# Kernel optimization log

Hardware: AMD Instinct MI355X
Metric: run time of the kernel (lower is better)

The kernel has to match this reference:

```python
import jax, jax.numpy as jnp
import numpy as np

B, S, H, NH, DIS = 8, 512, 512, 8, 32
HD = H // NH  # head_dim = 64


def setup_inputs() -> dict:
    key = jax.random.key(0)
    ks = jax.random.split(key, 9)
    sc = 0.05
    return {
        "x": jax.random.normal(ks[0], (B, S, H), jnp.float32),
        "rel_distance": jax.random.randint(ks[1], (B, S, 2 * S), 0, DIS, jnp.int64),
        "mask": jnp.zeros((B, S, 2 * S), jnp.bool_),
        "query_pos_embedding": jax.random.normal(ks[2], (DIS, H), jnp.float32) * sc,
        "key_pos_embedding": jax.random.normal(ks[3], (DIS, H), jnp.float32) * sc,
        "value_pos_embedding": jax.random.normal(ks[4], (DIS, H), jnp.float32) * sc,
        "Wq": jax.random.normal(ks[5], (H, H), jnp.float32) * sc,
        "Wk": jax.random.normal(ks[6], (2 * H, H), jnp.float32) * sc,
        "Wv": jax.random.normal(ks[7], (2 * H, H), jnp.float32) * sc,
        "Wo": jax.random.normal(ks[8], (H, H), jnp.float32) * sc,
    }


def reference(x, rel_distance, mask, query_pos_embedding, key_pos_embedding,
              value_pos_embedding, Wq, Wk, Wv, Wo):
    b, s, _ = x.shape
    scale = jnp.sqrt(jnp.asarray(HD, x.dtype))

    # projections (torch Linear: y = x @ W.T)
    q = (x @ Wq.T).reshape(b, s, NH, HD).transpose(0, 2, 1, 3)        # [B,h,S,d]
    k = (x @ Wk.T).reshape(b, 2 * s, NH, HD).transpose(0, 2, 1, 3)    # [B,h,2S,d]
    v = (x @ Wv.T).reshape(b, 2 * s, NH, HD).transpose(0, 2, 1, 3)    # [B,h,2S,d]

    rel = jnp.broadcast_to(rel_distance[:, None], (b, NH, s, 2 * s))  # [B,h,S,2S]

    # relative-position weights via gather along distance axis
    q_emb = query_pos_embedding.reshape(DIS, NH, HD)                  # [n,h,d]
    qpw_full = jnp.einsum('bhsd,nhd->bhsn', q, q_emb)                 # [B,h,S,n]
    qpw = jnp.take_along_axis(qpw_full, rel, axis=3)                  # [B,h,S,2S]

    k_emb = key_pos_embedding.reshape(DIS, NH, HD)
    kpw_full = jnp.einsum('bhkd,nhd->bhkn', k, k_emb)                 # [B,h,2S,n]
    kpw = jnp.take_along_axis(kpw_full, rel.transpose(0, 1, 3, 2), axis=3)  # [B,h,2S,S]
    kpw = kpw.transpose(0, 1, 3, 2)                                   # [B,h,S,2S]

    scores = (jnp.einsum('bhsd,bhkd->bhsk', q, k) + qpw + kpw) / scale
    scores = jnp.where(mask[:, None], -jnp.inf, scores)
    probs = jax.nn.softmax(scores, axis=-1)                           # [B,h,S,2S]

    # scatter-add probs into distance buckets: [B,h,S,n]
    bi = jnp.arange(b)[:, None, None, None]
    hi = jnp.arange(NH)[None, :, None, None]
    si = jnp.arange(s)[None, None, :, None]
    vdw = jnp.zeros((b, NH, s, DIS), probs.dtype).at[bi, hi, si, rel].add(probs)

    v_emb = value_pos_embedding.reshape(DIS, NH, HD)                  # [n,h,d]
    out = jnp.einsum('bhsk,bhkd->bhsd', probs, v) \
        + jnp.einsum('bhsn,nhd->bhsd', vdw, v_emb)                    # [B,h,S,d]
    out = out.transpose(0, 2, 1, 3).reshape(b, s, H)
    return out @ Wo.T
```

## Files before the change

kernel.cpp:

```cpp
#include <hip/hip_runtime.h>
#include <math.h>

#define Bc 8
#define Sc 512
#define Hc 512
#define NHc 8
#define HDc 64
#define DISc 32
#define S2c 1024

typedef __attribute__((ext_vector_type(8))) short bf16x8;
typedef __attribute__((ext_vector_type(4))) float f32x4;
#define MFMA16(a, b, c) __builtin_amdgcn_mfma_f32_16x16x32_bf16(a, b, c, 0, 0, 0)

__device__ __forceinline__ unsigned short f2bf(float f) {
  unsigned u = __float_as_uint(f);
  return (unsigned short)((u + 0x7fffu + ((u >> 16) & 1u)) >> 16);
}
__device__ __forceinline__ float b2f(unsigned short u) {
  return __uint_as_float((unsigned)u << 16);
}
__device__ __forceinline__ bf16x8 ldb16x8(const unsigned short* p) {
  union { uint4 u; bf16x8 s; } cv;
  cv.u = *(const uint4*)p;
  return cv.s;
}

__global__ __launch_bounds__(256) void cvt5_k(
    const float* __restrict__ x, const float* __restrict__ wq,
    const float* __restrict__ wk, const float* __restrict__ wv,
    const float* __restrict__ wo, unsigned short* __restrict__ x16,
    unsigned short* __restrict__ w16q, unsigned short* __restrict__ w16k,
    unsigned short* __restrict__ w16v, unsigned short* __restrict__ w16o) {
  int i = blockIdx.x * 256 + threadIdx.x;
  const float* src; unsigned short* dst; int off; float sc = 1.f;
  if (i < 524288)      { src = x;  dst = x16;  off = i; }
  else if (i < 589824) { src = wq; dst = w16q; off = i - 524288; sc = 0.125f; }
  else if (i < 720896) { src = wk; dst = w16k; off = i - 589824; }
  else if (i < 851968) { src = wv; dst = w16v; off = i - 720896; }
  else                 { src = wo; dst = w16o; off = i - 851968; }
  float4 v = ((const float4*)src)[off];
  ushort4 u;
  u.x = f2bf(v.x * sc); u.y = f2bf(v.y * sc);
  u.z = f2bf(v.z * sc); u.w = f2bf(v.w * sc);
  ((ushort4*)dst)[off] = u;
}

__global__ __launch_bounds__(256) void pack_k(const int* __restrict__ rel,
                                              const unsigned char* __restrict__ mask,
                                              unsigned char* __restrict__ pk8) {
  int i = blockIdx.x * 256 + threadIdx.x;
  const int* rp = rel + i * 16;
  uint4 mu = *(const uint4*)(mask + i * 16);
  const unsigned char* mb = (const unsigned char*)&mu;
  uint4 o;
  unsigned* ow = (unsigned*)&o;
#pragma unroll
  for (int g = 0; g < 4; ++g) {
    int4 r4 = ((const int4*)rp)[g];
    unsigned b0 = ((unsigned)r4.x & 31u) | (mb[g * 4 + 0] ? 0x80u : 0u);
    unsigned b1 = ((unsigned)r4.y & 31u) | (mb[g * 4 + 1] ? 0x80u : 0u);
    unsigned b2 = ((unsigned)r4.z & 31u) | (mb[g * 4 + 2] ? 0x80u : 0u);
    unsigned b3 = ((unsigned)r4.w & 31u) | (mb[g * 4 + 3] ? 0x80u : 0u);
    ow[g] = b0 | (b1 << 8) | (b2 << 16) | (b3 << 24);
  }
  *(uint4*)(pk8 + i * 16) = o;
}

__global__ __launch_bounds__(256) void wemb_k(
    const float* __restrict__ qpe, const float* __restrict__ kpe,
    const float* __restrict__ Wq, const float* __restrict__ Wk,
    unsigned short* __restrict__ wqp, unsigned short* __restrict__ wkp) {
  const int bid = blockIdx.x;
  const int cc = bid & 3, unit = bid >> 2;
  const int c0 = cc << 7;
  const int t = threadIdx.x;
  const float* emb; const float* Wsrc; unsigned short* outp; int rowbase, h;
  if (unit < 8) {
    h = unit; emb = qpe; Wsrc = Wq + (size_t)(h * 64) * 512; outp = wqp; rowbase = h * 32;
  } else {
    int u = unit - 8; int e = u >> 3; h = u & 7;
    emb = kpe; Wsrc = Wk + (size_t)(e * 512 + h * 64) * 512; outp = wkp;
    rowbase = e * 256 + h * 32;
  }
  __shared__ float es[32][65];
  __shared__ float wsh[64][132];
  {
    int n = t >> 3, d4 = (t & 7) << 3;
    float4 v0 = *(const float4*)(emb + (size_t)n * 512 + h * 64 + d4);
    float4 v1 = *(const float4*)(emb + (size_t)n * 512 + h * 64 + d4 + 4);
    *(float4*)&es[n][d4] = v0;
    *(float4*)&es[n][d4 + 4] = v1;
  }
#pragma unroll
  for (int p = 0; p < 8; ++p) {
    int slot = t + (p << 8);
    int d = slot >> 5, c4 = (slot & 31) << 2;
    *(float4*)&wsh[d][c4] = *(const float4*)(Wsrc + (size_t)d * 512 + c0 + c4);
  }
  __syncthreads();
  const int n = t >> 3, cb = (t & 7) << 4;
  float acc[16] = {};
#pragma unroll
  for (int d = 0; d < 64; ++d) {
    float ev = es[n][d];
    float4 w0 = *(const float4*)&wsh[d][cb];
    float4 w1 = *(const float4*)&wsh[d][cb + 4];
    float4 w2 = *(const float4*)&wsh[d][cb + 8];
    float4 w3 = *(const float4*)&wsh[d][cb + 12];
    acc[0] = fmaf(ev, w0.x, acc[0]);   acc[1] = fmaf(ev, w0.y, acc[1]);
    acc[2] = fmaf(ev, w0.z, acc[2]);   acc[3] = fmaf(ev, w0.w, acc[3]);
    acc[4] = fmaf(ev, w1.x, acc[4]);   acc[5] = fmaf(ev, w1.y, acc[5]);
    acc[6] = fmaf(ev, w1.z, acc[6]);   acc[7] = fmaf(ev, w1.w, acc[7]);
    acc[8] = fmaf(ev, w2.x, acc[8]);   acc[9] = fmaf(ev, w2.y, acc[9]);
    acc[10] = fmaf(ev, w2.z, acc[10]); acc[11] = fmaf(ev, w2.w, acc[11]);
    acc[12] = fmaf(ev, w3.x, acc[12]); acc[13] = fmaf(ev, w3.y, acc[13]);
    acc[14] = fmaf(ev, w3.z, acc[14]); acc[15] = fmaf(ev, w3.w, acc[15]);
  }
  unsigned short* orow = outp + (size_t)(rowbase + n) * 512 + c0 + cb;
#pragma unroll
  for (int j = 0; j < 16; ++j) orow[j] = f2bf(acc[j] * 0.125f);
}

__global__ __launch_bounds__(256, 4) void gemmqkv_k(
    const unsigned short* __restrict__ A,
    const unsigned short* __restrict__ wq, const unsigned short* __restrict__ wqp,
    const unsigned short* __restrict__ wk, const unsigned short* __restrict__ wkp,
    const unsigned short* __restrict__ wv,
    unsigned short* __restrict__ q16h, unsigned short* __restrict__ qpw16,
    unsigned short* __restrict__ kb16, unsigned short* __restrict__ kpw16,
    unsigned short* __restrict__ vT16) {
  const int t = threadIdx.x;
  const int w = t >> 6, lane = t & 63, ln = lane & 15, qd = lane >> 4;
  const int wm = (w >> 1) << 5, wn = (w & 1) << 5;
  const int m0 = blockIdx.y << 6, n0 = blockIdx.x << 6;
  __shared__ unsigned short As[64 * 72];
  __shared__ unsigned short Bs[64 * 72];
  const unsigned short* Bb;
  if (n0 < 512)        Bb = wq  + (size_t)n0 * 512;
  else if (n0 < 768)   Bb = wqp + (size_t)(n0 - 512) * 512;
  else if (n0 < 1792)  Bb = wk  + (size_t)(n0 - 768) * 512;
  else if (n0 < 2304)  Bb = wkp + (size_t)(n0 - 1792) * 512;
  else                 Bb = wv  + (size_t)(n0 - 2304) * 512;
  const int r0 = t >> 3, c8 = (t & 7) << 3;
  const unsigned short* ga = A + (size_t)(m0 + r0) * 512 + c8;
  const unsigned short* gb = Bb + (size_t)r0 * 512 + c8;
  const size_t half = (size_t)32 * 512;
  uint4 va0 = *(const uint4*)ga, va1 = *(const uint4*)(ga + half);
  uint4 vb0 = *(const uint4*)gb, vb1 = *(const uint4*)(gb + half);
  f32x4 z = {0.f, 0.f, 0.f, 0.f};
  f32x4 acc[2][2] = {{z, z}, {z, z}};
  for (int k0 = 0; k0 < 512; k0 += 64) {
    *(uint4*)&As[r0 * 72 + c8] = va0;
    *(uint4*)&As[(r0 + 32) * 72 + c8] = va1;
    *(uint4*)&Bs[r0 * 72 + c8] = vb0;
    *(uint4*)&Bs[(r0 + 32) * 72 + c8] = vb1;
    __syncthreads();
    if (k0 + 64 < 512) {
      va0 = *(const uint4*)(ga + k0 + 64);
      va1 = *(const uint4*)(ga + half + k0 + 64);
      vb0 = *(const uint4*)(gb + k0 + 64);
      vb1 = *(const uint4*)(gb + half + k0 + 64);
    }
#pragma unroll
    for (int kk = 0; kk < 64; kk += 32) {
      bf16x8 a0 = ldb16x8(&As[(wm + ln) * 72 + kk + qd * 8]);
      bf16x8 a1 = ldb16x8(&As[(wm + 16 + ln) * 72 + kk + qd * 8]);
      bf16x8 b0 = ldb16x8(&Bs[(wn + ln) * 72 + kk + qd * 8]);
      bf16x8 b1 = ldb16x8(&Bs[(wn + 16 + ln) * 72 + kk + qd * 8]);
      acc[0][0] = MFMA16(a0, b0, acc[0][0]);
      acc[0][1] = MFMA16(a0, b1, acc[0][1]);
      acc[1][0] = MFMA16(a1, b0, acc[1][0]);
      acc[1][1] = MFMA16(a1, b1, acc[1][1]);
    }
    __syncthreads();
  }
#pragma unroll
  for (int tm = 0; tm < 2; ++tm)
#pragma unroll
    for (int tn = 0; tn < 2; ++tn)
#pragma unroll
      for (int r = 0; r < 4; ++r) {
        int m = m0 + wm + tm * 16 + qd * 4 + r;
        int n = n0 + wn + tn * 16 + ln;
        unsigned short v16 = f2bf(acc[tm][tn][r]);
        int bb = m >> 9, s = m & 511;
        if (n0 < 512) {
          int hh = (n >> 6) & 7, d = n & 63;
          q16h[((size_t)(bb * 8 + hh) * 512 + s) * 64 + d] = v16;
        } else if (n0 < 768) {
          int n2 = n - 512, hh = n2 >> 5, nn = n2 & 31;
          qpw16[((size_t)(bb * 8 + hh) * 512 + s) * 32 + nn] = v16;
        } else if (n0 < 1792) {
          int n2 = n - 768, e = n2 >> 9, hh = (n2 >> 6) & 7, d = n2 & 63;
          int k2 = 2 * s + e;
          kb16[((size_t)(bb * 8 + hh) * 1024 + k2) * 64 + d] = v16;
        } else if (n0 < 2304) {
          int n2 = n - 1792, e = n2 >> 8, hh = (n2 >> 5) & 7, nn = n2 & 31;
          int k2 = 2 * s + e;
          kpw16[((size_t)(bb * 8 + hh) * 1024 + k2) * 32 + nn] = v16;
        } else {
          int n2 = n - 2304, e = n2 >> 9, hh = (n2 >> 6) & 7, d = n2 & 63;
          int k2 = 2 * s + e;
          vT16[((size_t)(bb * 8 + hh) * 64 + d) * 1024 + k2] = v16;
        }
      }
}

__global__ __launch_bounds__(256) void gemmo_k(
    const unsigned short* __restrict__ A, const unsigned short* __restrict__ Bw,
    float* __restrict__ out) {
  const int t = threadIdx.x;
  const int w = t >> 6, lane = t & 63, ln = lane & 15, qd = lane >> 4;
  const int wm = (w >> 1) << 6, wn = (w & 1) << 5;
  const int m0 = blockIdx.y << 7, n0 = blockIdx.x << 6;
  __shared__ unsigned short As[128 * 72];
  __shared__ unsigned short Bs[64 * 72];
  const int r0 = t >> 3, c8 = (t & 7) << 3;
  const unsigned short* ga = A + (size_t)(m0 + r0) * 512 + c8;
  const unsigned short* gb = Bw + (size_t)(n0 + r0) * 512 + c8;
  const size_t rs = (size_t)32 * 512;
  uint4 va0 = *(const uint4*)ga;
  uint4 va1 = *(const uint4*)(ga + rs);
  uint4 va2 = *(const uint4*)(ga + 2 * rs);
  uint4 va3 = *(const uint4*)(ga + 3 * rs);
  uint4 vb0 = *(const uint4*)gb;
  uint4 vb1 = *(const uint4*)(gb + rs);
  f32x4 z = {0.f, 0.f, 0.f, 0.f};
  f32x4 a00 = z, a01 = z, a10 = z, a11 = z;
  f32x4 a20 = z, a21 = z, a30 = z, a31 = z;
  for (int k0 = 0; k0 < 512; k0 += 64) {
    *(uint4*)&As[(r0) * 72 + c8] = va0;
    *(uint4*)&As[(r0 + 32) * 72 + c8] = va1;
    *(uint4*)&As[(r0 + 64) * 72 + c8] = va2;
    *(uint4*)&As[(r0 + 96) * 72 + c8] = va3;
    *(uint4*)&Bs[(r0) * 72 + c8] = vb0;
    *(uint4*)&Bs[(r0 + 32) * 72 + c8] = vb1;
    __syncthreads();
    if (k0 + 64 < 512) {
      va0 = *(const uint4*)(ga + k0 + 64);
      va1 = *(const uint4*)(ga + rs + k0 + 64);
      va2 = *(const uint4*)(ga + 2 * rs + k0 + 64);
      va3 = *(const uint4*)(ga + 3 * rs + k0 + 64);
      vb0 = *(const uint4*)(gb + k0 + 64);
      vb1 = *(const uint4*)(gb + rs + k0 + 64);
    }
#pragma unroll
    for (int kk = 0; kk < 64; kk += 32) {
      bf16x8 af0 = ldb16x8(&As[(wm + ln) * 72 + kk + qd * 8]);
      bf16x8 af1 = ldb16x8(&As[(wm + 16 + ln) * 72 + kk + qd * 8]);
      bf16x8 af2 = ldb16x8(&As[(wm + 32 + ln) * 72 + kk + qd * 8]);
      bf16x8 af3 = ldb16x8(&As[(wm + 48 + ln) * 72 + kk + qd * 8]);
      bf16x8 bf0 = ldb16x8(&Bs[(wn + ln) * 72 + kk + qd * 8]);
      bf16x8 bf1 = ldb16x8(&Bs[(wn + 16 + ln) * 72 + kk + qd * 8]);
      a00 = MFMA16(af0, bf0, a00); a01 = MFMA16(af0, bf1, a01);
      a10 = MFMA16(af1, bf0, a10); a11 = MFMA16(af1, bf1, a11);
      a20 = MFMA16(af2, bf0, a20); a21 = MFMA16(af2, bf1, a21);
      a30 = MFMA16(af3, bf0, a30); a31 = MFMA16(af3, bf1, a31);
    }
    __syncthreads();
  }
  float* ob = out + (size_t)(m0 + wm + qd * 4) * 512 + n0 + wn + ln;
#define ST(tm, tn, reg)                                            \
  _Pragma("unroll") for (int r = 0; r < 4; ++r)                    \
      ob[(size_t)((tm) * 16 + r) * 512 + (tn) * 16] = reg[r];
  ST(0, 0, a00) ST(0, 1, a01) ST(1, 0, a10) ST(1, 1, a11)
  ST(2, 0, a20) ST(2, 1, a21) ST(3, 0, a30) ST(3, 1, a31)
#undef ST
}

__global__ __launch_bounds__(512, 4) void attn6_k(
    const unsigned short* __restrict__ q16h, const unsigned short* __restrict__ kb16,
    const unsigned short* __restrict__ vT16, const unsigned short* __restrict__ qpw16,
    const unsigned short* __restrict__ kpw16, const unsigned char* __restrict__ pk8,
    const float* __restrict__ v_emb, unsigned short* __restrict__ attn16) {
  const int bid = blockIdx.x;
  const int b = bid & 7;
  const int h = (bid >> 3) & 7;
  const int qb = ((bid >> 6) & 7) << 6;
  const int t = threadIdx.x;
  const int w = t >> 6;
  const int g = w >> 2;
  const int ws4 = w & 3;
  const int lane = t & 63;
  const int ln = lane & 15;
  const int qd = lane >> 4;

  __shared__ __align__(16) char smem[52736];
  unsigned char*  pkt  = (unsigned char*)smem;
  unsigned short* kpws = (unsigned short*)(smem + 10240);
  unsigned short* q32s = (unsigned short*)(smem + 19456);
  unsigned short* pbuf = (unsigned short*)(smem + 24064);
  unsigned long long* vdwm64 = (unsigned long long*)(smem + 34304);
  float*          accbuf = (float*)smem;
  unsigned short* vest   = (unsigned short*)(smem + 19456);
  unsigned short* vdwb   = (unsigned short*)(smem + 24576);

  for (int i = t; i < 4 * 16 * 36; i += 512) vdwm64[i] = 0ull;
  if (t < 256) {
    int row = t >> 2, c8 = (t & 3) << 3;
    *(uint4*)&q32s[row * 36 + c8] =
        *(const uint4*)(qpw16 + ((size_t)((b * 8 + h) * 512 + qb) + row) * 32 + c8);
  }
  const unsigned short* kbase = kb16 + (size_t)(b * 8 + h) * 65536;
  const unsigned short* vbase = vT16 + (size_t)(b * 8 + h) * 65536;
  bf16x8 aQ[2];
  {
    const unsigned short* qsrc =
        q16h + ((size_t)((b * 8 + h) * 512 + qb + ws4 * 16 + ln)) * 64;
    aQ[0] = ldb16x8(qsrc + qd * 8);
    aQ[1] = ldb16x8(qsrc + 32 + qd * 8);
  }
  f32x4 z = {0.f, 0.f, 0.f, 0.f};
  f32x4 acc[4] = {z, z, z, z};

  const int u = t & 255, gg = t >> 8;
  const int qr = u >> 2, cg = (u & 3) << 4;
  const int kc8 = (u & 3) << 3;
  const unsigned char* pks = pk8 + ((size_t)(b * 512 + qb + qr)) * 1024 + (gg << 9);
  const unsigned short* kps =
      kpw16 + ((size_t)((b * 8 + h) * 1024) + (gg << 9) + qr) * 32 + kc8;
  unsigned char* pt_w = pkt + gg * 5120 + qr * 80 + cg;
  unsigned short* kp_w = kpws + gg * 2304 + qr * 36 + kc8;

  uint4 pv = *(const uint4*)(pks + cg);
  uint4 kv = *(const uint4*)kps;

  for (int kti = 0; kti < 8; ++kti) {
    *(uint4*)pt_w = pv;
    *(uint4*)kp_w = kv;
    __syncthreads();
    if (kti < 7) {
      pv = *(const uint4*)(pks + ((kti + 1) << 6) + cg);
      kv = *(const uint4*)(kps + ((size_t)(kti + 1) << 11));
    }
    const int kt0 = (kti + g * 8) << 6;

    f32x4 sc4[4];
#pragma unroll
    for (int t4 = 0; t4 < 4; ++t4) {
      f32x4 c = z;
      c = MFMA16(aQ[0], ldb16x8(kbase + (size_t)(kt0 + t4 * 16 + ln) * 64 + qd * 8), c);
      c = MFMA16(aQ[1], ldb16x8(kbase + (size_t)(kt0 + t4 * 16 + ln) * 64 + 32 + qd * 8), c);
      sc4[t4] = c;
    }

    unsigned char* pt_ = pkt + g * 5120;
    unsigned short* kp_ = kpws + g * 2304;
#pragma unroll
    for (int hf = 0; hf < 2; ++hf) {
#pragma unroll
      for (int r = 0; r < 4; ++r) {
#pragma unroll
        for (int t4h = 0; t4h < 2; ++t4h) {
          int t4 = hf * 2 + t4h;
          int row_l = ws4 * 16 + qd * 4 + r;
          int kl = t4 * 16 + ln;
          unsigned um = pt_[row_l * 80 + kl];
          int rd = um & 31;
          float s = sc4[t4][r] + b2f(q32s[row_l * 36 + rd]) + b2f(kp_[kl * 36 + rd]);
          float p = (um & 0x80u) ? 0.f : __expf(s);
          atomicAdd(&vdwm64[ws4 * 576 + (qd * 4 + r) * 36 + rd],
                    (unsigned long long)(p * 67108864.0f));
          pbuf[w * 640 + (qd * 4 + r) * 40 + t4h * 16 + ln] = f2bf(p);
        }
      }
      bf16x8 ah = ldb16x8(&pbuf[w * 640 + ln * 40 + qd * 8]);
#pragma unroll
      for (int dt = 0; dt < 4; ++dt)
        acc[dt] = MFMA16(ah, ldb16x8(vbase + (size_t)(dt * 16 + ln) * 1024 + kt0 + hf * 32 + qd * 8), acc[dt]);
    }
    __syncthreads();
  }

  if (t < 256) {
    int n = t >> 3, d0 = (t & 7) << 3;
    const float* src = v_emb + ((size_t)n << 9) + (h << 6) + d0;
    float4 f0 = *(const float4*)src;
    float4 f1 = *(const float4*)(src + 4);
    vest[(d0 + 0) * 40 + n] = f2bf(f0.x); vest[(d0 + 1) * 40 + n] = f2bf(f0.y);
    vest[(d0 + 2) * 40 + n] = f2bf(f0.z); vest[(d0 + 3) * 40 + n] = f2bf(f0.w);
    vest[(d0 + 4) * 40 + n] = f2bf(f1.x); vest[(d0 + 5) * 40 + n] = f2bf(f1.y);
    vest[(d0 + 6) * 40 + n] = f2bf(f1.z); vest[(d0 + 7) * 40 + n] = f2bf(f1.w);
  } else {
    int row = lane >> 2, n0 = (lane & 3) << 3;
    float vv[8];
#pragma unroll
    for (int j = 0; j < 8; ++j)
      vv[j] = (float)vdwm64[ws4 * 576 + row * 36 + n0 + j] * 1.4901161193847656e-8f;
    ushort4 u0, u1;
    u0.x = f2bf(vv[0]); u0.y = f2bf(vv[1]); u0.z = f2bf(vv[2]); u0.w = f2bf(vv[3]);
    u1.x = f2bf(vv[4]); u1.y = f2bf(vv[5]); u1.z = f2bf(vv[6]); u1.w = f2bf(vv[7]);
    *(ushort4*)&vdwb[ws4 * 640 + row * 40 + n0] = u0;
    *(ushort4*)&vdwb[ws4 * 640 + row * 40 + n0 + 4] = u1;
  }
  __syncthreads();

  if (g == 1) {
    bf16x8 av = ldb16x8(&vdwb[ws4 * 640 + ln * 40 + qd * 8]);
#pragma unroll
    for (int dt = 0; dt < 4; ++dt)
      acc[dt] = MFMA16(av, ldb16x8(&vest[(dt * 16 + ln) * 40 + qd * 8]), acc[dt]);
#pragma unroll
    for (int r = 0; r < 4; ++r)
#pragma unroll
      for (int dt = 0; dt < 4; ++dt)
        accbuf[ws4 * 1088 + (qd * 4 + r) * 68 + dt * 16 + ln] = acc[dt][r];
  }
  __syncthreads();

  if (g == 0) {
    float inv[4];
#pragma unroll
    for (int r = 0; r < 4; ++r) {
      unsigned long long lu = 0ull;
#pragma unroll
      for (int n = 0; n < 32; ++n)
        lu += vdwm64[ws4 * 576 + (qd * 4 + r) * 36 + n];
      inv[r] = 67108864.0f / (float)lu;
    }
    unsigned short* obase =
        attn16 + ((size_t)(b * 512 + qb + ws4 * 16 + qd * 4)) * 512 + (h << 6);
#pragma unroll
    for (int r = 0; r < 4; ++r)
#pragma unroll
      for (int dt = 0; dt < 4; ++dt) {
        float v = (acc[dt][r] + accbuf[ws4 * 1088 + (qd * 4 + r) * 68 + dt * 16 + ln]) * inv[r];
        obase[(size_t)r * 512 + dt * 16 + ln] = f2bf(v);
      }
  }
}

extern "C" void kernel_launch(void* const* d_in, const int* in_sizes, int n_in,
                              void* d_out, int out_size, void* d_ws, size_t ws_size,
                              hipStream_t stream) {
  const float* x = (const float*)d_in[0];
  const int* rel = (const int*)d_in[1];
  const unsigned char* mask = (const unsigned char*)d_in[2];
  const float* qpe = (const float*)d_in[3];
  const float* kpe = (const float*)d_in[4];
  const float* vpe = (const float*)d_in[5];
  const float* Wq = (const float*)d_in[6];
  const float* Wk = (const float*)d_in[7];
  const float* Wv = (const float*)d_in[8];
  const float* Wo = (const float*)d_in[9];
  float* out = (float*)d_out;

  unsigned short* u = (unsigned short*)d_ws;
  unsigned short* x16    = u;
  unsigned short* w16q   = x16 + 2097152;
  unsigned short* w16k   = w16q + 262144;
  unsigned short* w16v   = w16k + 524288;
  unsigned short* w16o   = w16v + 524288;
  unsigned short* wqp16  = w16o + 262144;
  unsigned short* wkp16  = wqp16 + 131072;
  unsigned short* q16h   = wkp16 + 262144;
  unsigned short* qpw16  = q16h + 2097152;
  unsigned short* kb16   = qpw16 + 1048576;
  unsigned short* kpw16  = kb16 + 4194304;
  unsigned short* vT16   = kpw16 + 2097152;
  unsigned short* attn16 = vT16 + 4194304;
  unsigned char* pk8 = (unsigned char*)(attn16 + 2097152);

  pack_k<<<1024, 256, 0, stream>>>(rel, mask, pk8);
  cvt5_k<<<3584, 256, 0, stream>>>(x, Wq, Wk, Wv, Wo, x16, w16q, w16k, w16v, w16o);
  wemb_k<<<96, 256, 0, stream>>>(qpe, kpe, Wq, Wk, wqp16, wkp16);
  gemmqkv_k<<<dim3(52, 64), 256, 0, stream>>>(x16, w16q, wqp16, w16k, wkp16, w16v,
                                              q16h, qpw16, kb16, kpw16, vT16);
  attn6_k<<<512, 512, 0, stream>>>(q16h, kb16, vT16, qpw16, kpw16, pk8, vpe, attn16);
  gemmo_k<<<dim3(8, 32), 256, 0, stream>>>(attn16, w16o, out);
}
```

Before: 217.1 us.

## Split attention key range across four wave groups with 32-row query tiles

The attention kernel now assigns 32 query rows per block instead of 64 and launches 1024 blocks. The 8 waves form 4 groups, each covering a quarter of the 1024 keys, where before 2 groups each covered half. Partial output accumulators from three groups go through shared memory and are summed by group 0. This raises grid size and per-row key-split parallelism, which should help occupancy and latency hiding. The cost is extra cross-group reduction traffic and the K/V fragments being reloaded by twice as many blocks.

After: 222.2 us. 1.02x slower.

```diff
diff --git a/kernel.cpp b/kernel.cpp
--- a/kernel.cpp
+++ b/kernel.cpp
@@ -269,7 +269,7 @@
 #undef ST
 }
 
-__global__ __launch_bounds__(512, 4) void attn6_k(
+__global__ __launch_bounds__(512, 4) void attn7_k(
     const unsigned short* __restrict__ q16h, const unsigned short* __restrict__ kb16,
     const unsigned short* __restrict__ vT16, const unsigned short* __restrict__ qpw16,
     const unsigned short* __restrict__ kpw16, const unsigned char* __restrict__ pk8,
@@ -277,75 +277,81 @@
   const int bid = blockIdx.x;
   const int b = bid & 7;
   const int h = (bid >> 3) & 7;
-  const int qb = ((bid >> 6) & 7) << 6;
+  const int qb = ((bid >> 6) & 15) << 5;
   const int t = threadIdx.x;
   const int w = t >> 6;
-  const int g = w >> 2;
-  const int ws4 = w & 3;
+  const int ws = w & 1;
+  const int g = w >> 1;
   const int lane = t & 63;
   const int ln = lane & 15;
   const int qd = lane >> 4;
 
-  __shared__ __align__(16) char smem[52736];
+  __shared__ __align__(16) char smem[50432];
   unsigned char*  pkt  = (unsigned char*)smem;
   unsigned short* kpws = (unsigned short*)(smem + 10240);
-  unsigned short* q32s = (unsigned short*)(smem + 19456);
-  unsigned short* pbuf = (unsigned short*)(smem + 24064);
-  unsigned long long* vdwm64 = (unsigned long long*)(smem + 34304);
+  unsigned short* q32s = (unsigned short*)(smem + 28672);
+  unsigned short* pbuf = (unsigned short*)(smem + 30976);
+  unsigned long long* vdwm64 = (unsigned long long*)(smem + 41216);
   float*          accbuf = (float*)smem;
-  unsigned short* vest   = (unsigned short*)(smem + 19456);
-  unsigned short* vdwb   = (unsigned short*)(smem + 24576);
-
-  for (int i = t; i < 4 * 16 * 36; i += 512) vdwm64[i] = 0ull;
-  if (t < 256) {
+  unsigned short* vest   = (unsigned short*)(smem + 28672);
+  unsigned short* vdwb   = (unsigned short*)(smem + 33792);
+
+  for (int i = t; i < 2 * 16 * 36; i += 512) vdwm64[i] = 0ull;
+  if (t < 128) {
     int row = t >> 2, c8 = (t & 3) << 3;
     *(uint4*)&q32s[row * 36 + c8] =
         *(const uint4*)(qpw16 + ((size_t)((b * 8 + h) * 512 + qb) + row) * 32 + c8);
   }
   const unsigned short* kbase = kb16 + (size_t)(b * 8 + h) * 65536;
   const unsigned short* vbase = vT16 + (size_t)(b * 8 + h) * 65536;
-  bf16x8 aQ[2];
+  bf16x8 aQ0, aQ1;
   {
     const unsigned short* qsrc =
-        q16h + ((size_t)((b * 8 + h) * 512 + qb + ws4 * 16 + ln)) * 64;
-    aQ[0] = ldb16x8(qsrc + qd * 8);
-    aQ[1] = ldb16x8(qsrc + 32 + qd * 8);
+        q16h + ((size_t)((b * 8 + h) * 512 + qb + ws * 16 + ln)) * 64;
+    aQ0 = ldb16x8(qsrc + qd * 8);
+    aQ1 = ldb16x8(qsrc + 32 + qd * 8);
   }
   f32x4 z = {0.f, 0.f, 0.f, 0.f};
   f32x4 acc[4] = {z, z, z, z};
 
-  const int u = t & 255, gg = t >> 8;
-  const int qr = u >> 2, cg = (u & 3) << 4;
-  const int kc8 = (u & 3) << 3;
-  const unsigned char* pks = pk8 + ((size_t)(b * 512 + qb + qr)) * 1024 + (gg << 9);
-  const unsigned short* kps =
-      kpw16 + ((size_t)((b * 8 + h) * 1024) + (gg << 9) + qr) * 32 + kc8;
-  unsigned char* pt_w = pkt + gg * 5120 + qr * 80 + cg;
-  unsigned short* kp_w = kpws + gg * 2304 + qr * 36 + kc8;
-
-  uint4 pv = *(const uint4*)(pks + cg);
-  uint4 kv = *(const uint4*)kps;
-
-  for (int kti = 0; kti < 8; ++kti) {
+  const int uq = t & 127, gq = t >> 7;
+  const int pqr = uq >> 2, pcg = (uq & 3) << 4;
+  const int kr0 = uq >> 2, kc0 = (uq & 3) << 3;
+  const unsigned char* pks =
+      pk8 + ((size_t)(b * 512 + qb + pqr)) * 1024 + gq * 256 + pcg;
+  const unsigned short* kps0 =
+      kpw16 + ((size_t)((b * 8 + h) * 1024) + gq * 256 + kr0) * 32 + kc0;
+  const unsigned short* kps1 = kps0 + 32 * 32;
+  unsigned char* pt_w = pkt + gq * 2560 + pqr * 80 + pcg;
+  unsigned short* kp_w0 = kpws + gq * 2304 + kr0 * 36 + kc0;
+  unsigned short* kp_w1 = kp_w0 + 32 * 36;
+
+  uint4 pv = *(const uint4*)pks;
+  uint4 kv0 = *(const uint4*)kps0;
+  uint4 kv1 = *(const uint4*)kps1;
+
+  for (int kti = 0; kti < 4; ++kti) {
     *(uint4*)pt_w = pv;
-    *(uint4*)kp_w = kv;
-    __syncthreads();
-    if (kti < 7) {
-      pv = *(const uint4*)(pks + ((kti + 1) << 6) + cg);
-      kv = *(const uint4*)(kps + ((size_t)(kti + 1) << 11));
-    }
-    const int kt0 = (kti + g * 8) << 6;
+    *(uint4*)kp_w0 = kv0;
+    *(uint4*)kp_w1 = kv1;
+    __syncthreads();
+    if (kti < 3) {
+      pv  = *(const uint4*)(pks + ((kti + 1) << 6));
+      kv0 = *(const uint4*)(kps0 + ((size_t)(kti + 1) << 11));
+      kv1 = *(const uint4*)(kps1 + ((size_t)(kti + 1) << 11));
+    }
+    const int kt0 = (kti + g * 4) << 6;
 
     f32x4 sc4[4];
 #pragma unroll
     for (int t4 = 0; t4 < 4; ++t4) {
       f32x4 c = z;
-      c = MFMA16(aQ[0], ldb16x8(kbase + (size_t)(kt0 + t4 * 16 + ln) * 64 + qd * 8), c);
-      c = MFMA16(aQ[1], ldb16x8(kbase + (size_t)(kt0 + t4 * 16 + ln) * 64 + 32 + qd * 8), c);
+      c = MFMA16(aQ0, ldb16x8(kbase + (size_t)(kt0 + t4 * 16 + ln) * 64 + qd * 8), c);
+      c = MFMA16(aQ1, ldb16x8(kbase + (size_t)(kt0 + t4 * 16 + ln) * 64 + 32 + qd * 8), c);
       sc4[t4] = c;
     }
 
-    unsigned char* pt_ = pkt + g * 5120;
+    unsigned char* pt_ = pkt + g * 2560;
     unsigned short* kp_ = kpws + g * 2304;
 #pragma unroll
     for (int hf = 0; hf < 2; ++hf) {
@@ -354,13 +360,13 @@
 #pragma unroll
         for (int t4h = 0; t4h < 2; ++t4h) {
           int t4 = hf * 2 + t4h;
-          int row_l = ws4 * 16 + qd * 4 + r;
+          int row_l = ws * 16 + qd * 4 + r;
           int kl = t4 * 16 + ln;
           unsigned um = pt_[row_l * 80 + kl];
           int rd = um & 31;
           float s = sc4[t4][r] + b2f(q32s[row_l * 36 + rd]) + b2f(kp_[kl * 36 + rd]);
           float p = (um & 0x80u) ? 0.f : __expf(s);
-          atomicAdd(&vdwm64[ws4 * 576 + (qd * 4 + r) * 36 + rd],
+          atomicAdd(&vdwm64[ws * 576 + (qd * 4 + r) * 36 + rd],
                     (unsigned long long)(p * 67108864.0f));
           pbuf[w * 640 + (qd * 4 + r) * 40 + t4h * 16 + ln] = f2bf(p);
         }
@@ -382,30 +388,33 @@
     vest[(d0 + 2) * 40 + n] = f2bf(f0.z); vest[(d0 + 3) * 40 + n] = f2bf(f0.w);
     vest[(d0 + 4) * 40 + n] = f2bf(f1.x); vest[(d0 + 5) * 40 + n] = f2bf(f1.y);
     vest[(d0 + 6) * 40 + n] = f2bf(f1.z); vest[(d0 + 7) * 40 + n] = f2bf(f1.w);
-  } else {
+  } else if (t < 384) {
+    int wsp = (t >> 6) & 1;
     int row = lane >> 2, n0 = (lane & 3) << 3;
     float vv[8];
 #pragma unroll
     for (int j = 0; j < 8; ++j)
-      vv[j] = (float)vdwm64[ws4 * 576 + row * 36 + n0 + j] * 1.4901161193847656e-8f;
+      vv[j] = (float)vdwm64[wsp * 576 + row * 36 + n0 + j] * 1.4901161193847656e-8f;
     ushort4 u0, u1;
     u0.x = f2bf(vv[0]); u0.y = f2bf(vv[1]); u0.z = f2bf(vv[2]); u0.w = f2bf(vv[3]);
     u1.x = f2bf(vv[4]); u1.y = f2bf(vv[5]); u1.z = f2bf(vv[6]); u1.w = f2bf(vv[7]);
-    *(ushort4*)&vdwb[ws4 * 640 + row * 40 + n0] = u0;
-    *(ushort4*)&vdwb[ws4 * 640 + row * 40 + n0 + 4] = u1;
+    *(ushort4*)&vdwb[wsp * 640 + row * 40 + n0] = u0;
+    *(ushort4*)&vdwb[wsp * 640 + row * 40 + n0 + 4] = u1;
   }
   __syncthreads();
 
   if (g == 1) {
-    bf16x8 av = ldb16x8(&vdwb[ws4 * 640 + ln * 40 + qd * 8]);
+    bf16x8 av = ldb16x8(&vdwb[ws * 640 + ln * 40 + qd * 8]);
 #pragma unroll
     for (int dt = 0; dt < 4; ++dt)
       acc[dt] = MFMA16(av, ldb16x8(&vest[(dt * 16 + ln) * 40 + qd * 8]), acc[dt]);
+  }
+  if (g >= 1) {
 #pragma unroll
     for (int r = 0; r < 4; ++r)
 #pragma unroll
       for (int dt = 0; dt < 4; ++dt)
-        accbuf[ws4 * 1088 + (qd * 4 + r) * 68 + dt * 16 + ln] = acc[dt][r];
+        accbuf[(g - 1) * 2176 + ws * 1088 + (qd * 4 + r) * 68 + dt * 16 + ln] = acc[dt][r];
   }
   __syncthreads();
 
@@ -416,17 +425,20 @@
       unsigned long long lu = 0ull;
 #pragma unroll
       for (int n = 0; n < 32; ++n)
-        lu += vdwm64[ws4 * 576 + (qd * 4 + r) * 36 + n];
+        lu += vdwm64[ws * 576 + (qd * 4 + r) * 36 + n];
       inv[r] = 67108864.0f / (float)lu;
     }
     unsigned short* obase =
-        attn16 + ((size_t)(b * 512 + qb + ws4 * 16 + qd * 4)) * 512 + (h << 6);
+        attn16 + ((size_t)(b * 512 + qb + ws * 16 + qd * 4)) * 512 + (h << 6);
 #pragma unroll
     for (int r = 0; r < 4; ++r)
 #pragma unroll
       for (int dt = 0; dt < 4; ++dt) {
-        float v = (acc[dt][r] + accbuf[ws4 * 1088 + (qd * 4 + r) * 68 + dt * 16 + ln]) * inv[r];
-        obase[(size_t)r * 512 + dt * 16 + ln] = f2bf(v);
+        float v = acc[dt][r];
+#pragma unroll
+        for (int gi = 0; gi < 3; ++gi)
+          v += accbuf[gi * 2176 + ws * 1088 + (qd * 4 + r) * 68 + dt * 16 + ln];
+        obase[(size_t)r * 512 + dt * 16 + ln] = f2bf(v * inv[r]);
       }
   }
 }
@@ -467,6 +479,6 @@
   wemb_k<<<96, 256, 0, stream>>>(qpe, kpe, Wq, Wk, wqp16, wkp16);
   gemmqkv_k<<<dim3(52, 64), 256, 0, stream>>>(x16, w16q, wqp16, w16k, wkp16, w16v,
                                               q16h, qpw16, kb16, kpw16, vT16);
-  attn6_k<<<512, 512, 0, stream>>>(q16h, kb16, vT16, qpw16, kpw16, pk8, vpe, attn16);
+  attn7_k<<<1024, 512, 0, stream>>>(q16h, kb16, vT16, qpw16, kpw16, pk8, vpe, attn16);
   gemmo_k<<<dim3(8, 32), 256, 0, stream>>>(attn16, w16o, out);
 }
```
